# Kernel tuning notes

Measured on AMD Instinct MI355X. Metric: run time of the kernel, lower is better.

## Reference

```python
import jax, jax.numpy as jnp
import numpy as np

NUM_JOINTS = 21
WINDOW = 131072  # window_size; pose3d has WINDOW+1 frames
N_BONES = NUM_JOINTS - 1
W_PROJ, W_BONE, W_SMOOTH, W_LIFT = 1.0, 1.0, 0.5, 0.1


def setup_inputs() -> dict:
    key = jax.random.key(0)
    k1, k2, k3, k4, k5 = jax.random.split(key, 5)
    pose3d = jax.random.normal(k1, (WINDOW + 1, 3, NUM_JOINTS), dtype=jnp.float32)
    camera_proj = jax.random.normal(k2, (WINDOW, 2, 3), dtype=jnp.float32)
    pose_2d = jax.random.normal(k3, (WINDOW, 2, NUM_JOINTS), dtype=jnp.float32)
    bone_lengths = jax.random.uniform(k4, (N_BONES,), dtype=jnp.float32)
    lift_directions = jax.random.normal(k5, (WINDOW, 3, N_BONES), dtype=jnp.float32)
    # normalize lift directions to unit vectors (they are bone directions)
    lift_directions = lift_directions / jnp.linalg.norm(lift_directions, axis=1, keepdims=True)
    # kinematic-chain bone connections: (child, parent) = (i+1, i), guaranteed distinct
    child = jnp.arange(1, NUM_JOINTS, dtype=jnp.int32)
    parent = jnp.arange(0, NUM_JOINTS - 1, dtype=jnp.int32)
    bone_connections = jnp.stack([child, parent], axis=1)  # [N_BONES, 2]
    lift_bone_connections = bone_connections
    return {
        "pose3d": pose3d,
        "camera_proj": camera_proj,
        "pose_2d": pose_2d,
        "bone_lengths": bone_lengths,
        "lift_directions": lift_directions,
        "bone_connections": bone_connections,
        "lift_bone_connections": lift_bone_connections,
    }


def reference(pose3d, camera_proj, pose_2d, bone_lengths, lift_directions,
              bone_connections, lift_bone_connections):
    J = NUM_JOINTS
    # --- projection loss: per-frame 2x3 camera applied to frames 1: ---
    projected = jnp.einsum('wij,wjk->wik', camera_proj, pose3d[1:])  # [W,2,J]
    proj_loss = jnp.sum(jnp.square(projected - pose_2d)) / (2 * J)
    # --- bone length loss ---
    d = pose3d[:, :, bone_connections[:, 0]] - pose3d[:, :, bone_connections[:, 1]]  # [W+1,3,NB]
    length_of_bone = jnp.sum(jnp.square(d), axis=1)  # [W+1, NB]
    bone_loss = jnp.sum(jnp.square(length_of_bone - bone_lengths[None, :])) / (J - 1)
    # --- smoothness loss (second difference) ---
    vel = pose3d[1:] - pose3d[:-1]  # [W,3,J]
    smooth_loss = jnp.sum(jnp.square(vel[1:] - vel[:-1])) / (3 * J)
    # --- lift direction loss ---
    bv = pose3d[1:, :, lift_bone_connections[:, 0]] - pose3d[1:, :, lift_bone_connections[:, 1]]  # [W,3,NB]
    norm = jnp.linalg.norm(bv, axis=1, keepdims=True)  # [W,1,NB]
    est_dirs = bv / norm
    lift_loss = jnp.sum(jnp.square(lift_directions - est_dirs)) / (3 * J)
    return (W_PROJ * proj_loss + W_BONE * bone_loss
            + W_SMOOTH * smooth_loss + W_LIFT * lift_loss)
```

## Files before the change

### kernel.cpp

```cpp
#include <hip/hip_runtime.h>
#include <math.h>

#define W 131072
#define FR 63
#define FPB 32
#define BLKT 128
#define NBLOCKS (W / FPB)
#define STG4 520
#define SMOOTH_TOT ((W - 1) * FR)

__global__ __launch_bounds__(BLKT) void loss_pass1(
    const float* __restrict__ pose3d,
    const float* __restrict__ cam,
    const float* __restrict__ p2d,
    const float* __restrict__ blen,
    const float* __restrict__ ldir,
    const int* __restrict__ bcon,
    const int* __restrict__ lcon,
    float* __restrict__ partial)
{
  __shared__ float sP[STG4 * 4];
  __shared__ float sWave[2];

  const int tid = threadIdx.x;
  const int blk = blockIdx.x;
  const int f0 = blk * FPB;
  const float* src = pose3d + (size_t)f0 * FR;

  {
    float4* s4 = (float4*)sP;
    const float4* g4 = (const float4*)src;
#pragma unroll
    for (int it = 0; it < 5; ++it) {
      int q = tid + it * BLKT;
      if (q < STG4) s4[q] = g4[q];
    }
  }

  float acc_smooth = 0.0f;
  {
    const int lim = (blk == NBLOCKS - 1) ? (SMOOTH_TOT - f0 * FR) : (FPB * FR);
#pragma unroll
    for (int g = 0; g < 4; ++g) {
      int o = tid * 16 + 4 * g;
      if (o + 4 <= lim) {
        float4 A = *(const float4*)(src + o);
        float4 B = *(const float4*)(src + o + 63);
        float4 C = *(const float4*)(src + o + 126);
        float dx = C.x - 2.0f * B.x + A.x;
        float dy = C.y - 2.0f * B.y + A.y;
        float dz = C.z - 2.0f * B.z + A.z;
        float dw = C.w - 2.0f * B.w + A.w;
        acc_smooth += dx * dx + dy * dy + dz * dz + dw * dw;
      } else {
#pragma unroll
        for (int e = 0; e < 4; ++e) {
          int oo = o + e;
          if (oo < lim) {
            float d2 = src[oo + 126] - 2.0f * src[oo + 63] + src[oo];
            acc_smooth += d2 * d2;
          }
        }
      }
    }
  }
  __syncthreads();

  const int s  = tid & 3;
  const int fl = tid >> 2;
  const int w  = f0 + fl;
  const float* P1 = sP + (fl + 1) * FR;

  float acc_proj = 0.0f;
  {
    const float* cp = cam + (size_t)w * 6;
    float c00 = cp[0], c01 = cp[1], c02 = cp[2];
    float c10 = cp[3], c11 = cp[4], c12 = cp[5];
    const float* pr = p2d + (size_t)w * 42;
#pragma unroll
    for (int k = 0; k < 6; ++k) {
      int j = s + 4 * k;
      if (j < 21) {
        float x = P1[j], y = P1[21 + j], z = P1[42 + j];
        float d0 = c00 * x + c01 * y + c02 * z - pr[j];
        float d1 = c10 * x + c11 * y + c12 * z - pr[21 + j];
        acc_proj += d0 * d0 + d1 * d1;
      }
    }
  }

  float acc_bone = 0.0f, acc_lift = 0.0f;
  {
    const int2* bc2 = (const int2*)bcon;
    const int2* lc2 = (const int2*)lcon;
    const float* lr = ldir + (size_t)w * 60;
    float bl[5], lx[5], ly[5], lz[5];
    bool ch = true;
#pragma unroll
    for (int k = 0; k < 5; ++k) {
      int b = 5 * s + k;
      int2 lc = lc2[b];
      int2 bc = bc2[b];
      ch = ch && (lc.x == b + 1) && (lc.y == b) && (bc.x == b + 1) && (bc.y == b);
      bl[k] = blen[b];
      lx[k] = lr[b];
      ly[k] = lr[20 + b];
      lz[k] = lr[40 + b];
    }
    if (__all(ch)) {
      float Jx[6], Jy[6], Jz[6];
#pragma unroll
      for (int m = 0; m < 6; ++m) {
        int j = 5 * s + m;
        Jx[m] = P1[j]; Jy[m] = P1[21 + j]; Jz[m] = P1[42 + j];
      }
#pragma unroll
      for (int k = 0; k < 5; ++k) {
        float dx = Jx[k + 1] - Jx[k];
        float dy = Jy[k + 1] - Jy[k];
        float dz = Jz[k + 1] - Jz[k];
        float S = dx * dx + dy * dy + dz * dz;
        float inv = rsqrtf(S);
        float ex = lx[k] - dx * inv;
        float ey = ly[k] - dy * inv;
        float ez = lz[k] - dz * inv;
        acc_lift += ex * ex + ey * ey + ez * ez;
        float t = S - bl[k];
        acc_bone += t * t;
      }
    } else {
#pragma unroll
      for (int k = 0; k < 5; ++k) {
        int b = 5 * s + k;
        int2 lc = lc2[b];
        float dx = P1[lc.x]      - P1[lc.y];
        float dy = P1[21 + lc.x] - P1[21 + lc.y];
        float dz = P1[42 + lc.x] - P1[42 + lc.y];
        float S = dx * dx + dy * dy + dz * dz;
        float inv = rsqrtf(S);
        float ex = lx[k] - dx * inv;
        float ey = ly[k] - dy * inv;
        float ez = lz[k] - dz * inv;
        acc_lift += ex * ex + ey * ey + ez * ez;
        int2 bc = bc2[b];
        float Sb = S;
        if (bc.x != lc.x || bc.y != lc.y) {
          float bx = P1[bc.x]      - P1[bc.y];
          float by = P1[21 + bc.x] - P1[21 + bc.y];
          float bz = P1[42 + bc.x] - P1[42 + bc.y];
          Sb = bx * bx + by * by + bz * bz;
        }
        float t = Sb - bl[k];
        acc_bone += t * t;
      }
    }
    if (w == 0) {
      const float* P0 = sP;
#pragma unroll
      for (int k = 0; k < 5; ++k) {
        int b = 5 * s + k;
        int2 bc = bc2[b];
        float bx = P0[bc.x]      - P0[bc.y];
        float by = P0[21 + bc.x] - P0[21 + bc.y];
        float bz = P0[42 + bc.x] - P0[42 + bc.y];
        float Sb = bx * bx + by * by + bz * bz;
        float t = Sb - bl[k];
        acc_bone += t * t;
      }
    }
  }

  float tot = acc_proj * (1.0f / 42.0f) + acc_bone * (1.0f / 20.0f)
            + acc_smooth * (0.5f / 63.0f) + acc_lift * (0.1f / 63.0f);
#pragma unroll
  for (int off = 32; off > 0; off >>= 1) tot += __shfl_xor(tot, off, 64);
  if ((tid & 63) == 0) sWave[tid >> 6] = tot;
  __syncthreads();
  if (tid == 0) partial[blk] = sWave[0] + sWave[1];
}

__global__ __launch_bounds__(256) void loss_pass2(
    const float* __restrict__ partial, float* __restrict__ out)
{
  __shared__ float sW[4];
  int tid = threadIdx.x;
  float s = 0.0f;
#pragma unroll
  for (int i = 0; i < NBLOCKS / 256; ++i) s += partial[i * 256 + tid];
#pragma unroll
  for (int off = 32; off > 0; off >>= 1) s += __shfl_xor(s, off, 64);
  if ((tid & 63) == 0) sW[tid >> 6] = s;
  __syncthreads();
  if (tid == 0) {
    float t = 0.0f;
#pragma unroll
    for (int i = 0; i < 4; ++i) t += sW[i];
    out[0] = t;
  }
}

extern "C" void kernel_launch(void* const* d_in, const int* in_sizes, int n_in,
                              void* d_out, int out_size, void* d_ws, size_t ws_size,
                              hipStream_t stream) {
  const float* pose3d = (const float*)d_in[0];
  const float* cam    = (const float*)d_in[1];
  const float* p2d    = (const float*)d_in[2];
  const float* blen   = (const float*)d_in[3];
  const float* ldir   = (const float*)d_in[4];
  const int*   bcon   = (const int*)d_in[5];
  const int*   lcon   = (const int*)d_in[6];
  float* out     = (float*)d_out;
  float* partial = (float*)d_ws;

  loss_pass1<<<NBLOCKS, BLKT, 0, stream>>>(pose3d, cam, p2d, blen, ldir,
                                           bcon, lcon, partial);
  loss_pass2<<<1, 256, 0, stream>>>(partial, out);
}
```

Before: 130.3 us.

## Stage all per-frame inputs in LDS with padded pose pitch and compute smoothness from shared

Stages pose (34 frames at a padded 68-float pitch), 2D keypoints, lift directions and camera matrices into shared memory with coalesced float4 loads. The smoothness term now reads from shared instead of issuing overlapping global loads. The projection loop switches to contiguous joint ranges per thread. This is meant to cut redundant global traffic and uncoalesced per-thread global reads, at the cost of more LDS use per block, which may lower occupancy.

```diff
diff --git a/kernel.cpp b/kernel.cpp
--- a/kernel.cpp
+++ b/kernel.cpp
@@ -6,8 +6,8 @@
 #define FPB 32
 #define BLKT 128
 #define NBLOCKS (W / FPB)
-#define STG4 520
-#define SMOOTH_TOT ((W - 1) * FR)
+#define TFR 34
+#define PPITCH 68
 
 __global__ __launch_bounds__(BLKT) void loss_pass1(
     const float* __restrict__ pose3d,
@@ -19,68 +19,101 @@
     const int* __restrict__ lcon,
     float* __restrict__ partial)
 {
-  __shared__ float sP[STG4 * 4];
+  __shared__ float sPose[TFR * PPITCH];
+  __shared__ float sP2d[FPB * 42];
+  __shared__ float sLdir[FPB * 60];
+  __shared__ float sCam[FPB * 6];
   __shared__ float sWave[2];
 
   const int tid = threadIdx.x;
   const int blk = blockIdx.x;
   const int f0 = blk * FPB;
-  const float* src = pose3d + (size_t)f0 * FR;
-
-  {
-    float4* s4 = (float4*)sP;
-    const float4* g4 = (const float4*)src;
-#pragma unroll
-    for (int it = 0; it < 5; ++it) {
-      int q = tid + it * BLKT;
-      if (q < STG4) s4[q] = g4[q];
-    }
-  }
-
-  float acc_smooth = 0.0f;
-  {
-    const int lim = (blk == NBLOCKS - 1) ? (SMOOTH_TOT - f0 * FR) : (FPB * FR);
-#pragma unroll
-    for (int g = 0; g < 4; ++g) {
-      int o = tid * 16 + 4 * g;
-      if (o + 4 <= lim) {
-        float4 A = *(const float4*)(src + o);
-        float4 B = *(const float4*)(src + o + 63);
-        float4 C = *(const float4*)(src + o + 126);
-        float dx = C.x - 2.0f * B.x + A.x;
-        float dy = C.y - 2.0f * B.y + A.y;
-        float dz = C.z - 2.0f * B.z + A.z;
-        float dw = C.w - 2.0f * B.w + A.w;
-        acc_smooth += dx * dx + dy * dy + dz * dz + dw * dw;
-      } else {
-#pragma unroll
-        for (int e = 0; e < 4; ++e) {
-          int oo = o + e;
-          if (oo < lim) {
-            float d2 = src[oo + 126] - 2.0f * src[oo + 63] + src[oo];
-            acc_smooth += d2 * d2;
+
+  {
+    const float* src = pose3d + (size_t)f0 * FR;
+    const int m = tid & 15;
+    const int fi0 = tid >> 4;
+    if (blk != NBLOCKS - 1) {
+#pragma unroll
+      for (int r = 0; r < 5; ++r) {
+        int fi = fi0 + 8 * r;
+        if (fi < TFR) {
+          float4 v = *(const float4*)(src + 63 * fi + 4 * m);
+          *(float4*)(sPose + PPITCH * fi + 4 * m) = v;
+        }
+      }
+    } else {
+#pragma unroll
+      for (int r = 0; r < 5; ++r) {
+        int fi = fi0 + 8 * r;
+        if (fi <= 32) {
+          if (fi < 32 || m < 15) {
+            float4 v = *(const float4*)(src + 63 * fi + 4 * m);
+            *(float4*)(sPose + PPITCH * fi + 4 * m) = v;
+          } else {
+            sPose[PPITCH * 32 + 60] = src[63 * 32 + 60];
+            sPose[PPITCH * 32 + 61] = src[63 * 32 + 61];
+            sPose[PPITCH * 32 + 62] = src[63 * 32 + 62];
           }
         }
       }
     }
+  }
+  {
+    const float4* g = (const float4*)(p2d + (size_t)f0 * 42);
+    float4* d = (float4*)sP2d;
+#pragma unroll
+    for (int it = 0; it < 3; ++it) { int q = tid + it * BLKT; if (q < 336) d[q] = g[q]; }
+  }
+  {
+    const float4* g = (const float4*)(ldir + (size_t)f0 * 60);
+    float4* d = (float4*)sLdir;
+#pragma unroll
+    for (int it = 0; it < 4; ++it) { int q = tid + it * BLKT; if (q < 480) d[q] = g[q]; }
+  }
+  {
+    const float4* g = (const float4*)(cam + (size_t)f0 * 6);
+    float4* d = (float4*)sCam;
+    if (tid < 48) d[tid] = g[tid];
   }
   __syncthreads();
 
   const int s  = tid & 3;
   const int fl = tid >> 2;
   const int w  = f0 + fl;
-  const float* P1 = sP + (fl + 1) * FR;
+
+  float acc_smooth = 0.0f;
+  if (w < W - 1) {
+    const float* A = sPose + PPITCH * fl + 16 * s;
+    const float* B = A + PPITCH;
+    const float* C = B + PPITCH;
+#pragma unroll
+    for (int q = 0; q < 4; ++q) {
+      float4 a = *(const float4*)(A + 4 * q);
+      float4 b = *(const float4*)(B + 4 * q);
+      float4 c = *(const float4*)(C + 4 * q);
+      float dx = c.x - 2.0f * b.x + a.x;
+      float dy = c.y - 2.0f * b.y + a.y;
+      float dz = c.z - 2.0f * b.z + a.z;
+      float dw = c.w - 2.0f * b.w + a.w;
+      if (q == 3 && s == 3) dw = 0.0f;
+      acc_smooth += dx * dx + dy * dy + dz * dz + dw * dw;
+    }
+  }
+
+  const float* P1 = sPose + PPITCH * (fl + 1);
 
   float acc_proj = 0.0f;
   {
-    const float* cp = cam + (size_t)w * 6;
+    const float* cp = sCam + 6 * fl;
     float c00 = cp[0], c01 = cp[1], c02 = cp[2];
     float c10 = cp[3], c11 = cp[4], c12 = cp[5];
-    const float* pr = p2d + (size_t)w * 42;
+    const float* pr = sP2d + 42 * fl;
+    const int kend = (s == 3) ? 6 : 5;
 #pragma unroll
     for (int k = 0; k < 6; ++k) {
-      int j = s + 4 * k;
-      if (j < 21) {
+      if (k < kend) {
+        int j = 5 * s + k;
         float x = P1[j], y = P1[21 + j], z = P1[42 + j];
         float d0 = c00 * x + c01 * y + c02 * z - pr[j];
         float d1 = c10 * x + c11 * y + c12 * z - pr[21 + j];
@@ -91,58 +124,50 @@
 
   float acc_bone = 0.0f, acc_lift = 0.0f;
   {
+    const float* lr = sLdir + 60 * fl;
     const int2* bc2 = (const int2*)bcon;
     const int2* lc2 = (const int2*)lcon;
-    const float* lr = ldir + (size_t)w * 60;
-    float bl[5], lx[5], ly[5], lz[5];
+    int2 lcA[5], bcA[5];
+    float blA[5];
     bool ch = true;
 #pragma unroll
     for (int k = 0; k < 5; ++k) {
       int b = 5 * s + k;
-      int2 lc = lc2[b];
-      int2 bc = bc2[b];
-      ch = ch && (lc.x == b + 1) && (lc.y == b) && (bc.x == b + 1) && (bc.y == b);
-      bl[k] = blen[b];
-      lx[k] = lr[b];
-      ly[k] = lr[20 + b];
-      lz[k] = lr[40 + b];
+      lcA[k] = lc2[b]; bcA[k] = bc2[b]; blA[k] = blen[b];
+      ch = ch && lcA[k].x == b + 1 && lcA[k].y == b
+              && bcA[k].x == b + 1 && bcA[k].y == b;
     }
     if (__all(ch)) {
-      float Jx[6], Jy[6], Jz[6];
-#pragma unroll
-      for (int m = 0; m < 6; ++m) {
-        int j = 5 * s + m;
-        Jx[m] = P1[j]; Jy[m] = P1[21 + j]; Jz[m] = P1[42 + j];
-      }
 #pragma unroll
       for (int k = 0; k < 5; ++k) {
-        float dx = Jx[k + 1] - Jx[k];
-        float dy = Jy[k + 1] - Jy[k];
-        float dz = Jz[k + 1] - Jz[k];
+        int b = 5 * s + k;
+        float dx = P1[b + 1]      - P1[b];
+        float dy = P1[21 + b + 1] - P1[21 + b];
+        float dz = P1[42 + b + 1] - P1[42 + b];
         float S = dx * dx + dy * dy + dz * dz;
         float inv = rsqrtf(S);
-        float ex = lx[k] - dx * inv;
-        float ey = ly[k] - dy * inv;
-        float ez = lz[k] - dz * inv;
+        float ex = lr[b]      - dx * inv;
+        float ey = lr[20 + b] - dy * inv;
+        float ez = lr[40 + b] - dz * inv;
         acc_lift += ex * ex + ey * ey + ez * ez;
-        float t = S - bl[k];
+        float t = S - blA[k];
         acc_bone += t * t;
       }
     } else {
 #pragma unroll
       for (int k = 0; k < 5; ++k) {
         int b = 5 * s + k;
-        int2 lc = lc2[b];
+        int2 lc = lcA[k];
         float dx = P1[lc.x]      - P1[lc.y];
         float dy = P1[21 + lc.x] - P1[21 + lc.y];
         float dz = P1[42 + lc.x] - P1[42 + lc.y];
         float S = dx * dx + dy * dy + dz * dz;
         float inv = rsqrtf(S);
-        float ex = lx[k] - dx * inv;
-        float ey = ly[k] - dy * inv;
-        float ez = lz[k] - dz * inv;
+        float ex = lr[b]      - dx * inv;
+        float ey = lr[20 + b] - dy * inv;
+        float ez = lr[40 + b] - dz * inv;
         acc_lift += ex * ex + ey * ey + ez * ez;
-        int2 bc = bc2[b];
+        int2 bc = bcA[k];
         float Sb = S;
         if (bc.x != lc.x || bc.y != lc.y) {
           float bx = P1[bc.x]      - P1[bc.y];
@@ -150,21 +175,20 @@
           float bz = P1[42 + bc.x] - P1[42 + bc.y];
           Sb = bx * bx + by * by + bz * bz;
         }
-        float t = Sb - bl[k];
+        float t = Sb - blA[k];
         acc_bone += t * t;
       }
     }
-    if (w == 0) {
-      const float* P0 = sP;
+    if (blk == 0 && fl == 0) {
+      const float* P0 = sPose;
 #pragma unroll
       for (int k = 0; k < 5; ++k) {
-        int b = 5 * s + k;
-        int2 bc = bc2[b];
+        int2 bc = bcA[k];
         float bx = P0[bc.x]      - P0[bc.y];
         float by = P0[21 + bc.x] - P0[21 + bc.y];
         float bz = P0[42 + bc.x] - P0[42 + bc.y];
         float Sb = bx * bx + by * by + bz * bz;
-        float t = Sb - bl[k];
+        float t = Sb - blA[k];
         acc_bone += t * t;
       }
     }
```

New measurement: 131.6 us. No clear change (+1.0%).
